# Performance work log

Measured on AMD Instinct MI355X. Metric: run time of the kernel, lower is better.

Reference implementation:

```python
import jax, jax.numpy as jnp
import numpy as np

LN_EPS = 1e-5


def setup_inputs() -> dict:
    key = jax.random.key(0)
    ks = jax.random.split(key, 12)
    B, T, U, H, V = 4, 512, 128, 512, 41
    src = jax.random.normal(ks[0], (B, T, H), dtype=jnp.float32)
    tgt = jax.random.normal(ks[1], (B, U, H), dtype=jnp.float32)
    src_len = jax.random.randint(ks[2], (B,), 1, T + 1, dtype=jnp.int32)
    tgt_len = jax.random.randint(ks[3], (B,), 1, U + 1, dtype=jnp.int32)
    s = 1.0 / np.sqrt(H)
    W1 = jax.random.uniform(ks[4], (H, H), jnp.float32, -s, s)
    b1 = jax.random.uniform(ks[5], (H,), jnp.float32, -s, s)
    W2 = jax.random.uniform(ks[6], (H, H), jnp.float32, -s, s)
    b2 = jax.random.uniform(ks[7], (H,), jnp.float32, -s, s)
    ln_g = jnp.ones((H,), jnp.float32)
    ln_b = jnp.zeros((H,), jnp.float32)
    Wl = jax.random.uniform(ks[8], (H, V), jnp.float32, -s, s)
    bl = jax.random.uniform(ks[9], (V,), jnp.float32, -s, s)
    return dict(source_encodings=src, source_lengths=src_len,
                target_encodings=tgt, target_lengths=tgt_len,
                W1=W1, b1=b1, W2=W2, b2=b2, ln_g=ln_g, ln_b=ln_b,
                Wl=Wl, bl=bl)


def _f_target(tgt, W1, b1, W2, b2, ln_g, ln_b):
    h = jax.nn.gelu(tgt @ W1 + b1, approximate=False)  # exact GELU (torch default)
    h = h @ W2 + b2
    mu = jnp.mean(h, axis=-1, keepdims=True)
    var = jnp.var(h, axis=-1, keepdims=True)
    return (h - mu) * jax.lax.rsqrt(var + LN_EPS) * ln_g + ln_b


def reference(source_encodings, source_lengths, target_encodings, target_lengths,
              W1, b1, W2, b2, ln_g, ln_b, Wl, bl):
    tgt = _f_target(target_encodings, W1, b1, W2, b2, ln_g, ln_b)  # [B,U,H]
    # joint broadcast add: [B,T,1,H] + [B,1,U,H] -> [B,T,U,H]
    joint = source_encodings[:, :, None, :] + tgt[:, None, :, :]
    act = jnp.tanh(joint)
    out = act @ Wl + bl  # [B,T,U,V]
    return out, source_lengths, target_lengths
```

## Files before the change

kernel.cpp:

```cpp
#include <hip/hip_runtime.h>
#include <math.h>

#define Bb 4
#define Tt 512
#define Uu 128
#define Hh 512
#define Vv 41

typedef __attribute__((ext_vector_type(8))) short short8;
typedef __attribute__((ext_vector_type(4))) float f32x4;
typedef __attribute__((ext_vector_type(2))) float v2f;

__device__ __forceinline__ unsigned pack_bf16_rne(float hi, float lo) {
    unsigned xh = __float_as_uint(hi); xh += 0x7fffu + ((xh >> 16) & 1u);
    unsigned xl = __float_as_uint(lo); xl += 0x7fffu + ((xl >> 16) & 1u);
    return __builtin_amdgcn_perm(xh, xl, 0x07060302);
}

__device__ __forceinline__ unsigned short bf16_rne(float v) {
    unsigned x = __float_as_uint(v);
    x += 0x7fffu + ((x >> 16) & 1u);
    return (unsigned short)(x >> 16);
}

__device__ __forceinline__ unsigned tanh2_pack(float x0, float x1) {
    v2f xc;
    xc.x = __builtin_amdgcn_fmed3f(x0, -3.0f, 3.0f);
    xc.y = __builtin_amdgcn_fmed3f(x1, -3.0f, 3.0f);
    v2f t = xc * xc;
    v2f p = t * (v2f){-0.00140725f, -0.00140725f} + (v2f){0.0288922f, 0.0288922f};
    p = p * t + (v2f){-0.2177528f, -0.2177528f};
    p = p * t + (v2f){0.9707868f, 0.9707868f};
    v2f g = xc * p;
    return __builtin_amdgcn_perm(__float_as_uint(g.y), __float_as_uint(g.x), 0x07060302);
}

__global__ __launch_bounds__(256) void prep_pack(
    const float* __restrict__ W1, const float* __restrict__ W2,
    const float* __restrict__ Wl,
    unsigned short* __restrict__ Wp1, unsigned short* __restrict__ Wp2,
    unsigned short* __restrict__ Wpl,
    const int* __restrict__ sl, const int* __restrict__ tl,
    float* __restrict__ lenDst)
{
    __shared__ float T[64][65];
    const int bid = blockIdx.x, tid = threadIdx.x;

    if (bid == 135 && tid < 2 * Bb) {
        lenDst[tid] = (tid < Bb) ? (float)sl[tid] : (float)tl[tid - Bb];
    }

    const float* Wsrc; unsigned short* Wdst; int k0, n0, isWl;
    if (bid < 64)       { Wsrc = W1; Wdst = Wp1; k0 = (bid >> 3) * 64; n0 = (bid & 7) * 64; isWl = 0; }
    else if (bid < 128) { Wsrc = W2; Wdst = Wp2; k0 = ((bid - 64) >> 3) * 64; n0 = ((bid - 64) & 7) * 64; isWl = 0; }
    else                { Wsrc = Wl; Wdst = Wpl; k0 = (bid - 128) * 64; n0 = 0; isWl = 1; }

    #pragma unroll
    for (int i = 0; i < 16; ++i) {
        int idx = i * 256 + tid;
        int kk = idx >> 6, nn = idx & 63;
        float v;
        if (isWl) v = (nn < Vv) ? Wl[(k0 + kk) * Vv + nn] : 0.0f;
        else      v = Wsrc[(size_t)(k0 + kk) * 512 + n0 + nn];
        T[kk][nn] = v;
    }
    __syncthreads();

    #pragma unroll
    for (int i = 0; i < 2; ++i) {
        int task = i * 256 + tid;
        int nn = task & 63, kg = task >> 6;
        if (isWl && nn >= 48) continue;
        int n = n0 + nn, k = k0 + kg * 8;
        float e[8];
        #pragma unroll
        for (int j = 0; j < 8; ++j) e[j] = T[kg * 8 + j][nn];
        uint4 pk;
        pk.x = pack_bf16_rne(e[1], e[0]);
        pk.y = pack_bf16_rne(e[3], e[2]);
        pk.z = pack_bf16_rne(e[5], e[4]);
        pk.w = pack_bf16_rne(e[7], e[6]);
        int ntg = n >> 4, ncol = n & 15;
        int ks = (k >> 5) & 15, quad = (k >> 3) & 3;
        int lane = quad * 16 + ncol;
        *(uint4*)(Wdst + (size_t)((ntg * 16 + ks) * 64 + lane) * 8) = pk;
    }
}

__global__ __launch_bounds__(1024) void target_kernel(
    const float* __restrict__ tgt,
    const unsigned short* __restrict__ Wp1, const float* __restrict__ b1,
    const unsigned short* __restrict__ Wp2, const float* __restrict__ b2,
    const float* __restrict__ ln_g, const float* __restrict__ ln_b,
    float* __restrict__ tgtPf)
{
    __shared__ unsigned short At[16][520];
    __shared__ float Ct[16][516];

    const int tid = threadIdx.x;
    const int lane = tid & 63, wave = tid >> 6;
    const int ncol = lane & 15, quad = lane >> 4;
    const int r0 = blockIdx.x * 16;

    {
        const float4* t4 = (const float4*)(tgt + (size_t)r0 * Hh);
        #pragma unroll
        for (int j = 0; j < 2; ++j) {
            int fi = tid + j * 1024;
            int row = fi >> 7, c4 = fi & 127;
            float4 v = t4[fi];
            uint2 pk;
            pk.x = pack_bf16_rne(v.y, v.x);
            pk.y = pack_bf16_rne(v.w, v.z);
            *(uint2*)&At[row][c4 * 4] = pk;
        }
    }
    __syncthreads();

    f32x4 acc[2];
    acc[0] = (f32x4){0.f, 0.f, 0.f, 0.f};
    acc[1] = (f32x4){0.f, 0.f, 0.f, 0.f};

    const unsigned short* bp1 = Wp1 + (size_t)(wave * 2) * 8192 + lane * 8;
    const unsigned short* bp2 = Wp2 + (size_t)(wave * 2) * 8192 + lane * 8;

    {
        short8 cb0 = *(const short8*)(bp1);
        short8 cb1 = *(const short8*)(bp1 + 8192);
        #pragma unroll
        for (int ks = 0; ks < 16; ++ks) {
            short8 nb0, nb1;
            if (ks < 15) {
                nb0 = *(const short8*)(bp1 + (ks + 1) * 512);
                nb1 = *(const short8*)(bp1 + 8192 + (ks + 1) * 512);
            }
            short8 af = *(const short8*)&At[ncol][ks * 32 + quad * 8];
            acc[0] = __builtin_amdgcn_mfma_f32_16x16x32_bf16(af, cb0, acc[0], 0, 0, 0);
            acc[1] = __builtin_amdgcn_mfma_f32_16x16x32_bf16(af, cb1, acc[1], 0, 0, 0);
            cb0 = nb0; cb1 = nb1;
        }
    }
    __syncthreads();

    #pragma unroll
    for (int nt = 0; nt < 2; ++nt) {
        int n = wave * 32 + nt * 16 + ncol;
        float bias = b1[n];
        #pragma unroll
        for (int r = 0; r < 4; ++r) {
            float v = acc[nt][r] + bias;
            float g = 0.5f * v * (1.0f + erff(v * 0.70710678118654752f));
            At[quad * 4 + r][n] = bf16_rne(g);
        }
        acc[nt] = (f32x4){0.f, 0.f, 0.f, 0.f};
    }
    __syncthreads();

    {
        short8 cb0 = *(const short8*)(bp2);
        short8 cb1 = *(const short8*)(bp2 + 8192);
        #pragma unroll
        for (int ks = 0; ks < 16; ++ks) {
            short8 nb0, nb1;
            if (ks < 15) {
                nb0 = *(const short8*)(bp2 + (ks + 1) * 512);
                nb1 = *(const short8*)(bp2 + 8192 + (ks + 1) * 512);
            }
            short8 af = *(const short8*)&At[ncol][ks * 32 + quad * 8];
            acc[0] = __builtin_amdgcn_mfma_f32_16x16x32_bf16(af, cb0, acc[0], 0, 0, 0);
            acc[1] = __builtin_amdgcn_mfma_f32_16x16x32_bf16(af, cb1, acc[1], 0, 0, 0);
            cb0 = nb0; cb1 = nb1;
        }
    }

    #pragma unroll
    for (int nt = 0; nt < 2; ++nt) {
        int n = wave * 32 + nt * 16 + ncol;
        float bias = b2[n];
        #pragma unroll
        for (int r = 0; r < 4; ++r)
            Ct[quad * 4 + r][n] = acc[nt][r] + bias;
    }
    __syncthreads();

    {
        const int row = wave;
        const float2* cr2 = (const float2*)&Ct[row][0];
        float2 vv[4];
        float s = 0.f, q = 0.f;
        #pragma unroll
        for (int j = 0; j < 4; ++j) {
            float2 v = cr2[lane + 64 * j];
            vv[j] = v;
            s += v.x + v.y;
            q += v.x * v.x + v.y * v.y;
        }
        #pragma unroll
        for (int off = 32; off > 0; off >>= 1) {
            s += __shfl_xor(s, off, 64);
            q += __shfl_xor(q, off, 64);
        }
        float mu = s * (1.0f / Hh);
        float rs = rsqrtf(q * (1.0f / Hh) - mu * mu + 1e-5f);
        int r = r0 + row;
        int bb = r >> 7, u = r & 127;
        float* obase = tgtPf + (size_t)bb * 65536 + u * 8;
        #pragma unroll
        for (int j = 0; j < 4; ++j) {
            int k2 = lane + 64 * j;
            int k = k2 * 2;
            float2 g2 = ((const float2*)ln_g)[k2];
            float2 bv = ((const float2*)ln_b)[k2];
            float2 o;
            o.x = (vv[j].x - mu) * rs * g2.x + bv.x;
            o.y = (vv[j].y - mu) * rs * g2.y + bv.y;
            *(float2*)(obase + ((k >> 3) << 10) + (k & 7)) = o;
        }
    }
}

__global__ __launch_bounds__(256) void joint_mfma(
    const float* __restrict__ src, const float* __restrict__ tgtPf,
    const unsigned short* __restrict__ Wpl, const float* __restrict__ bl,
    float* __restrict__ out)
{
    __shared__ float srcl[2 * Hh];

    const int t0 = blockIdx.x * 2, b = blockIdx.y, uh = blockIdx.z;
    const int tid = threadIdx.x;
    const int lane = tid & 63, wave = tid >> 6;
    const int ncol = lane & 15, quad = lane >> 4;

    const float4* s4 = (const float4*)(src + ((size_t)(b * Tt + t0)) * Hh);
    ((float4*)srcl)[tid] = s4[tid];

    const int u0 = uh * 64 + (wave & 1) * 32 + ncol;
    const float* pA = tgtPf + (size_t)b * 65536 + u0 * 8;
    const unsigned short* bp = Wpl + lane * 8;

    float4 a0 = *(const float4*)(pA + quad * 1024);
    float4 a1 = *(const float4*)(pA + quad * 1024 + 4);
    float4 c0 = *(const float4*)(pA + quad * 1024 + 128);
    float4 c1 = *(const float4*)(pA + quad * 1024 + 132);

    float bln[3];
    #pragma unroll
    for (int nt = 0; nt < 3; ++nt) {
        int n = nt * 16 + ncol;
        bln[nt] = (n < Vv) ? bl[n] : 0.0f;
    }

    f32x4 acc[2][3];
    #pragma unroll
    for (int mi = 0; mi < 2; ++mi)
        #pragma unroll
        for (int nt = 0; nt < 3; ++nt)
            acc[mi][nt] = (f32x4){0.f, 0.f, 0.f, 0.f};

    __syncthreads();

    const float* srow = srcl + (wave >> 1) * Hh;

    #pragma unroll 4
    for (int ks = 0; ks < 16; ++ks) {
        float4 na0, na1, nc0, nc1;
        if (ks < 15) {
            const float* pn = pA + ((ks + 1) * 4 + quad) * 1024;
            na0 = *(const float4*)(pn);
            na1 = *(const float4*)(pn + 4);
            nc0 = *(const float4*)(pn + 128);
            nc1 = *(const float4*)(pn + 132);
        }
        const float* sp = srow + ks * 32 + quad * 8;
        float4 sA = *(const float4*)(sp);
        float4 sB = *(const float4*)(sp + 4);

        union { uint4 u; short8 s; } f0, f1;
        f0.u.x = tanh2_pack(sA.x + a0.x, sA.y + a0.y);
        f0.u.y = tanh2_pack(sA.z + a0.z, sA.w + a0.w);
        f0.u.z = tanh2_pack(sB.x + a1.x, sB.y + a1.y);
        f0.u.w = tanh2_pack(sB.z + a1.z, sB.w + a1.w);
        f1.u.x = tanh2_pack(sA.x + c0.x, sA.y + c0.y);
        f1.u.y = tanh2_pack(sA.z + c0.z, sA.w + c0.w);
        f1.u.z = tanh2_pack(sB.x + c1.x, sB.y + c1.y);
        f1.u.w = tanh2_pack(sB.z + c1.z, sB.w + c1.w);

        #pragma unroll
        for (int nt = 0; nt < 3; ++nt) {
            short8 bfr = *(const short8*)(bp + (nt * 16 + ks) * 512);
            acc[0][nt] = __builtin_amdgcn_mfma_f32_16x16x32_bf16(f0.s, bfr, acc[0][nt], 0, 0, 0);
            acc[1][nt] = __builtin_amdgcn_mfma_f32_16x16x32_bf16(f1.s, bfr, acc[1][nt], 0, 0, 0);
        }
        a0 = na0; a1 = na1; c0 = nc0; c1 = nc1;
    }

    const int t = t0 + (wave >> 1);
    const int ub = uh * 64 + (wave & 1) * 32;
    float* ob = out + ((size_t)(b * Tt + t)) * Uu * Vv;
    #pragma unroll
    for (int mi = 0; mi < 2; ++mi) {
        #pragma unroll
        for (int nt = 0; nt < 3; ++nt) {
            int n = nt * 16 + ncol;
            if (n < Vv) {
                #pragma unroll
                for (int r = 0; r < 4; ++r) {
                    int m = ub + mi * 16 + quad * 4 + r;
                    ob[m * Vv + n] = acc[mi][nt][r] + bln[nt];
                }
            }
        }
    }
}

extern "C" void kernel_launch(void* const* d_in, const int* in_sizes, int n_in,
                              void* d_out, int out_size, void* d_ws, size_t ws_size,
                              hipStream_t stream)
{
    const float* src  = (const float*)d_in[0];
    const int*   slen = (const int*)  d_in[1];
    const float* tgt  = (const float*)d_in[2];
    const int*   tlen = (const int*)  d_in[3];
    const float* W1   = (const float*)d_in[4];
    const float* b1   = (const float*)d_in[5];
    const float* W2   = (const float*)d_in[6];
    const float* b2   = (const float*)d_in[7];
    const float* ln_g = (const float*)d_in[8];
    const float* ln_b = (const float*)d_in[9];
    const float* Wl   = (const float*)d_in[10];
    const float* bl   = (const float*)d_in[11];

    float* out = (float*)d_out;
    float* tgtPf = (float*)d_ws;
    unsigned short* Wp1 = (unsigned short*)((char*)d_ws + 1048576);
    unsigned short* Wp2 = (unsigned short*)((char*)d_ws + 1048576 + 524288);
    unsigned short* Wpl = (unsigned short*)((char*)d_ws + 2097152);

    hipLaunchKernelGGL(prep_pack, dim3(136), dim3(256), 0, stream,
                       W1, W2, Wl, Wp1, Wp2, Wpl,
                       slen, tlen, out + (size_t)Bb * Tt * Uu * Vv);
    hipLaunchKernelGGL(target_kernel, dim3(Bb * Uu / 16), dim3(1024), 0, stream,
                       tgt, Wp1, b1, Wp2, b2, ln_g, ln_b, tgtPf);
    hipLaunchKernelGGL(joint_mfma, dim3(Tt / 2, Bb, 2), dim3(256), 0, stream,
                       src, tgtPf, Wpl, bl, out);
}
```

Measured before the change: 144.4 us.

## Split target MLP into parallel GEMM and layernorm kernels, prefetch joint operands

```diff
diff --git a/kernel.cpp b/kernel.cpp
--- a/kernel.cpp
+++ b/kernel.cpp
@@ -37,19 +37,45 @@
 
 __global__ __launch_bounds__(256) void prep_pack(
     const float* __restrict__ W1, const float* __restrict__ W2,
-    const float* __restrict__ Wl,
+    const float* __restrict__ Wl, const float* __restrict__ tgt,
     unsigned short* __restrict__ Wp1, unsigned short* __restrict__ Wp2,
-    unsigned short* __restrict__ Wpl,
+    unsigned short* __restrict__ Wpl, unsigned short* __restrict__ tgtA,
     const int* __restrict__ sl, const int* __restrict__ tl,
     float* __restrict__ lenDst)
 {
-    __shared__ float T[64][65];
+    __shared__ __align__(16) char smem[16640];
     const int bid = blockIdx.x, tid = threadIdx.x;
 
-    if (bid == 135 && tid < 2 * Bb) {
+    if (bid >= 136) {
+        unsigned short (*At)[520] = (unsigned short (*)[520])smem;
+        const int rt = bid - 136;
+        const float4* t4 = (const float4*)(tgt + (size_t)rt * 16 * Hh);
+        #pragma unroll
+        for (int j = 0; j < 8; ++j) {
+            int fi = j * 256 + tid;
+            int row = fi >> 7, c4 = fi & 127;
+            float4 v = t4[fi];
+            uint2 pk;
+            pk.x = pack_bf16_rne(v.y, v.x);
+            pk.y = pack_bf16_rne(v.w, v.z);
+            *(uint2*)&At[row][c4 * 4] = pk;
+        }
+        __syncthreads();
+        #pragma unroll
+        for (int i = 0; i < 4; ++i) {
+            int chunk = i * 256 + tid;
+            int ks = chunk >> 6, l = chunk & 63;
+            int q = l >> 4, nc = l & 15;
+            short8 v = *(const short8*)&At[nc][ks * 32 + q * 8];
+            *(short8*)(tgtA + ((size_t)(rt * 16 + ks) * 64 + l) * 8) = v;
+        }
+        return;
+    }
+
+    if (bid == 135 && tid < 2 * Bb)
         lenDst[tid] = (tid < Bb) ? (float)sl[tid] : (float)tl[tid - Bb];
-    }
-
+
+    float (*T)[65] = (float (*)[65])smem;
     const float* Wsrc; unsigned short* Wdst; int k0, n0, isWl;
     if (bid < 64)       { Wsrc = W1; Wdst = Wp1; k0 = (bid >> 3) * 64; n0 = (bid & 7) * 64; isWl = 0; }
     else if (bid < 128) { Wsrc = W2; Wdst = Wp2; k0 = ((bid - 64) >> 3) * 64; n0 = ((bid - 64) & 7) * 64; isWl = 0; }
@@ -87,136 +113,135 @@
     }
 }
 
-__global__ __launch_bounds__(1024) void target_kernel(
-    const float* __restrict__ tgt,
+__global__ __launch_bounds__(128) void gemm_t1(
+    const unsigned short* __restrict__ tgtA,
     const unsigned short* __restrict__ Wp1, const float* __restrict__ b1,
+    unsigned short* __restrict__ h1A)
+{
+    __shared__ unsigned short At[16][72];
+    const int nb = blockIdx.x, rt = blockIdx.y;
+    const int tid = threadIdx.x, lane = tid & 63, w = tid >> 6;
+    const int ncol = lane & 15, quad = lane >> 4;
+    const int nt0 = nb * 4 + w * 2;
+
+    const unsigned short* ap = tgtA + ((size_t)rt * 1024 + lane) * 8;
+    const unsigned short* bp = Wp1 + (size_t)lane * 8;
+
+    f32x4 acc0 = (f32x4){0.f,0.f,0.f,0.f}, acc1 = (f32x4){0.f,0.f,0.f,0.f};
+    short8 ac  = *(const short8*)(ap);
+    short8 b0c = *(const short8*)(bp + (size_t)nt0 * 8192);
+    short8 b1c = *(const short8*)(bp + (size_t)(nt0 + 1) * 8192);
+
+    #pragma unroll
+    for (int ks = 0; ks < 16; ++ks) {
+        short8 an, b0n, b1n;
+        if (ks < 15) {
+            an  = *(const short8*)(ap + (ks + 1) * 512);
+            b0n = *(const short8*)(bp + (size_t)nt0 * 8192 + (ks + 1) * 512);
+            b1n = *(const short8*)(bp + (size_t)(nt0 + 1) * 8192 + (ks + 1) * 512);
+        }
+        acc0 = __builtin_amdgcn_mfma_f32_16x16x32_bf16(ac, b0c, acc0, 0, 0, 0);
+        acc1 = __builtin_amdgcn_mfma_f32_16x16x32_bf16(ac, b1c, acc1, 0, 0, 0);
+        ac = an; b0c = b0n; b1c = b1n;
+    }
+
+    #pragma unroll
+    for (int nt = 0; nt < 2; ++nt) {
+        int n = nb * 64 + w * 32 + nt * 16 + ncol;
+        float bias = b1[n];
+        f32x4 A = nt ? acc1 : acc0;
+        #pragma unroll
+        for (int r = 0; r < 4; ++r) {
+            float v = A[r] + bias;
+            float g = 0.5f * v * (1.0f + erff(v * 0.70710678118654752f));
+            At[quad * 4 + r][w * 32 + nt * 16 + ncol] = bf16_rne(g);
+        }
+    }
+    __syncthreads();
+
+    {
+        int g2 = w, l = lane;
+        short8 v = *(const short8*)&At[l & 15][g2 * 32 + (l >> 4) * 8];
+        int ksg = nb * 2 + g2;
+        *(short8*)(h1A + ((size_t)(rt * 16 + ksg) * 64 + l) * 8) = v;
+    }
+}
+
+__global__ __launch_bounds__(128) void gemm_t2(
+    const unsigned short* __restrict__ h1A,
     const unsigned short* __restrict__ Wp2, const float* __restrict__ b2,
-    const float* __restrict__ ln_g, const float* __restrict__ ln_b,
-    float* __restrict__ tgtPf)
-{
-    __shared__ unsigned short At[16][520];
-    __shared__ float Ct[16][516];
-
-    const int tid = threadIdx.x;
-    const int lane = tid & 63, wave = tid >> 6;
+    float* __restrict__ h2)
+{
+    const int nb = blockIdx.x, rt = blockIdx.y;
+    const int tid = threadIdx.x, lane = tid & 63, w = tid >> 6;
     const int ncol = lane & 15, quad = lane >> 4;
-    const int r0 = blockIdx.x * 16;
-
-    {
-        const float4* t4 = (const float4*)(tgt + (size_t)r0 * Hh);
-        #pragma unroll
-        for (int j = 0; j < 2; ++j) {
-            int fi = tid + j * 1024;
-            int row = fi >> 7, c4 = fi & 127;
-            float4 v = t4[fi];
-            uint2 pk;
-            pk.x = pack_bf16_rne(v.y, v.x);
-            pk.y = pack_bf16_rne(v.w, v.z);
-            *(uint2*)&At[row][c4 * 4] = pk;
-        }
-    }
-    __syncthreads();
-
-    f32x4 acc[2];
-    acc[0] = (f32x4){0.f, 0.f, 0.f, 0.f};
-    acc[1] = (f32x4){0.f, 0.f, 0.f, 0.f};
-
-    const unsigned short* bp1 = Wp1 + (size_t)(wave * 2) * 8192 + lane * 8;
-    const unsigned short* bp2 = Wp2 + (size_t)(wave * 2) * 8192 + lane * 8;
-
-    {
-        short8 cb0 = *(const short8*)(bp1);
-        short8 cb1 = *(const short8*)(bp1 + 8192);
-        #pragma unroll
-        for (int ks = 0; ks < 16; ++ks) {
-            short8 nb0, nb1;
-            if (ks < 15) {
-                nb0 = *(const short8*)(bp1 + (ks + 1) * 512);
-                nb1 = *(const short8*)(bp1 + 8192 + (ks + 1) * 512);
-            }
-            short8 af = *(const short8*)&At[ncol][ks * 32 + quad * 8];
-            acc[0] = __builtin_amdgcn_mfma_f32_16x16x32_bf16(af, cb0, acc[0], 0, 0, 0);
-            acc[1] = __builtin_amdgcn_mfma_f32_16x16x32_bf16(af, cb1, acc[1], 0, 0, 0);
-            cb0 = nb0; cb1 = nb1;
-        }
-    }
-    __syncthreads();
+    const int nt0 = nb * 4 + w * 2;
+
+    const unsigned short* ap = h1A + ((size_t)rt * 1024 + lane) * 8;
+    const unsigned short* bp = Wp2 + (size_t)lane * 8;
+
+    f32x4 acc0 = (f32x4){0.f,0.f,0.f,0.f}, acc1 = (f32x4){0.f,0.f,0.f,0.f};
+    short8 ac  = *(const short8*)(ap);
+    short8 b0c = *(const short8*)(bp + (size_t)nt0 * 8192);
+    short8 b1c = *(const short8*)(bp + (size_t)(nt0 + 1) * 8192);
+
+    #pragma unroll
+    for (int ks = 0; ks < 16; ++ks) {
+        short8 an, b0n, b1n;
+        if (ks < 15) {
+            an  = *(const short8*)(ap + (ks + 1) * 512);
+            b0n = *(const short8*)(bp + (size_t)nt0 * 8192 + (ks + 1) * 512);
+            b1n = *(const short8*)(bp + (size_t)(nt0 + 1) * 8192 + (ks + 1) * 512);
+        }
+        acc0 = __builtin_amdgcn_mfma_f32_16x16x32_bf16(ac, b0c, acc0, 0, 0, 0);
+        acc1 = __builtin_amdgcn_mfma_f32_16x16x32_bf16(ac, b1c, acc1, 0, 0, 0);
+        ac = an; b0c = b0n; b1c = b1n;
+    }
 
     #pragma unroll
     for (int nt = 0; nt < 2; ++nt) {
-        int n = wave * 32 + nt * 16 + ncol;
-        float bias = b1[n];
-        #pragma unroll
-        for (int r = 0; r < 4; ++r) {
-            float v = acc[nt][r] + bias;
-            float g = 0.5f * v * (1.0f + erff(v * 0.70710678118654752f));
-            At[quad * 4 + r][n] = bf16_rne(g);
-        }
-        acc[nt] = (f32x4){0.f, 0.f, 0.f, 0.f};
-    }
-    __syncthreads();
-
-    {
-        short8 cb0 = *(const short8*)(bp2);
-        short8 cb1 = *(const short8*)(bp2 + 8192);
-        #pragma unroll
-        for (int ks = 0; ks < 16; ++ks) {
-            short8 nb0, nb1;
-            if (ks < 15) {
-                nb0 = *(const short8*)(bp2 + (ks + 1) * 512);
-                nb1 = *(const short8*)(bp2 + 8192 + (ks + 1) * 512);
-            }
-            short8 af = *(const short8*)&At[ncol][ks * 32 + quad * 8];
-            acc[0] = __builtin_amdgcn_mfma_f32_16x16x32_bf16(af, cb0, acc[0], 0, 0, 0);
-            acc[1] = __builtin_amdgcn_mfma_f32_16x16x32_bf16(af, cb1, acc[1], 0, 0, 0);
-            cb0 = nb0; cb1 = nb1;
-        }
-    }
-
-    #pragma unroll
-    for (int nt = 0; nt < 2; ++nt) {
-        int n = wave * 32 + nt * 16 + ncol;
+        int n = nb * 64 + w * 32 + nt * 16 + ncol;
         float bias = b2[n];
+        f32x4 A = nt ? acc1 : acc0;
         #pragma unroll
         for (int r = 0; r < 4; ++r)
-            Ct[quad * 4 + r][n] = acc[nt][r] + bias;
-    }
-    __syncthreads();
-
-    {
-        const int row = wave;
-        const float2* cr2 = (const float2*)&Ct[row][0];
-        float2 vv[4];
-        float s = 0.f, q = 0.f;
-        #pragma unroll
-        for (int j = 0; j < 4; ++j) {
-            float2 v = cr2[lane + 64 * j];
-            vv[j] = v;
-            s += v.x + v.y;
-            q += v.x * v.x + v.y * v.y;
-        }
-        #pragma unroll
-        for (int off = 32; off > 0; off >>= 1) {
-            s += __shfl_xor(s, off, 64);
-            q += __shfl_xor(q, off, 64);
-        }
-        float mu = s * (1.0f / Hh);
-        float rs = rsqrtf(q * (1.0f / Hh) - mu * mu + 1e-5f);
-        int r = r0 + row;
-        int bb = r >> 7, u = r & 127;
-        float* obase = tgtPf + (size_t)bb * 65536 + u * 8;
-        #pragma unroll
-        for (int j = 0; j < 4; ++j) {
-            int k2 = lane + 64 * j;
-            int k = k2 * 2;
-            float2 g2 = ((const float2*)ln_g)[k2];
-            float2 bv = ((const float2*)ln_b)[k2];
-            float2 o;
-            o.x = (vv[j].x - mu) * rs * g2.x + bv.x;
-            o.y = (vv[j].y - mu) * rs * g2.y + bv.y;
-            *(float2*)(obase + ((k >> 3) << 10) + (k & 7)) = o;
-        }
-    }
+            h2[(size_t)(rt * 16 + quad * 4 + r) * 512 + n] = A[r] + bias;
+    }
+}
+
+__global__ __launch_bounds__(256) void ln_kernel(
+    const float* __restrict__ h2, const float* __restrict__ ln_g,
+    const float* __restrict__ ln_b, float* __restrict__ tgtPf)
+{
+    const int r = blockIdx.x * 4 + (threadIdx.x >> 6);
+    const int lane = threadIdx.x & 63;
+    const float4* row4 = (const float4*)(h2 + (size_t)r * Hh);
+    float4 v0 = row4[lane], v1 = row4[lane + 64];
+    float s = v0.x + v0.y + v0.z + v0.w + v1.x + v1.y + v1.z + v1.w;
+    float q = v0.x*v0.x + v0.y*v0.y + v0.z*v0.z + v0.w*v0.w
+            + v1.x*v1.x + v1.y*v1.y + v1.z*v1.z + v1.w*v1.w;
+    #pragma unroll
+    for (int off = 32; off > 0; off >>= 1) {
+        s += __shfl_xor(s, off, 64);
+        q += __shfl_xor(q, off, 64);
+    }
+    float mu = s * (1.0f / Hh);
+    float rs = rsqrtf(q * (1.0f / Hh) - mu * mu + 1e-5f);
+
+    float4 g0 = ((const float4*)ln_g)[lane], g1 = ((const float4*)ln_g)[lane + 64];
+    float4 be0 = ((const float4*)ln_b)[lane], be1 = ((const float4*)ln_b)[lane + 64];
+    float4 o0, o1;
+    o0.x = (v0.x - mu) * rs * g0.x + be0.x;  o0.y = (v0.y - mu) * rs * g0.y + be0.y;
+    o0.z = (v0.z - mu) * rs * g0.z + be0.z;  o0.w = (v0.w - mu) * rs * g0.w + be0.w;
+    o1.x = (v1.x - mu) * rs * g1.x + be1.x;  o1.y = (v1.y - mu) * rs * g1.y + be1.y;
+    o1.z = (v1.z - mu) * rs * g1.z + be1.z;  o1.w = (v1.w - mu) * rs * g1.w + be1.w;
+
+    const int bb = r >> 7, u = r & 127;
+    float* ob = tgtPf + (size_t)bb * 65536 + u * 8;
+    int k0 = lane * 4;
+    *(float4*)(ob + (k0 >> 3) * 1024 + (k0 & 7)) = o0;
+    int k1 = lane * 4 + 256;
+    *(float4*)(ob + (k1 >> 3) * 1024 + (k1 & 7)) = o1;
 }
 
 __global__ __launch_bounds__(256) void joint_mfma(
@@ -236,44 +261,47 @@
 
     const int u0 = uh * 64 + (wave & 1) * 32 + ncol;
     const float* pA = tgtPf + (size_t)b * 65536 + u0 * 8;
-    const unsigned short* bp = Wpl + lane * 8;
+    const unsigned short* bp = Wpl + (size_t)lane * 8;
 
     float4 a0 = *(const float4*)(pA + quad * 1024);
     float4 a1 = *(const float4*)(pA + quad * 1024 + 4);
     float4 c0 = *(const float4*)(pA + quad * 1024 + 128);
     float4 c1 = *(const float4*)(pA + quad * 1024 + 132);
-
-    float bln[3];
+    short8 B0 = *(const short8*)(bp);
+    short8 B1 = *(const short8*)(bp + 8192);
+    short8 B2 = *(const short8*)(bp + 16384);
+
+    f32x4 acc[2][3];
     #pragma unroll
     for (int nt = 0; nt < 3; ++nt) {
         int n = nt * 16 + ncol;
-        bln[nt] = (n < Vv) ? bl[n] : 0.0f;
-    }
-
-    f32x4 acc[2][3];
-    #pragma unroll
-    for (int mi = 0; mi < 2; ++mi)
-        #pragma unroll
-        for (int nt = 0; nt < 3; ++nt)
-            acc[mi][nt] = (f32x4){0.f, 0.f, 0.f, 0.f};
+        float bv = (n < Vv) ? bl[n] : 0.0f;
+        acc[0][nt] = (f32x4){bv, bv, bv, bv};
+        acc[1][nt] = (f32x4){bv, bv, bv, bv};
+    }
 
     __syncthreads();
-
     const float* srow = srcl + (wave >> 1) * Hh;
+    float4 sA = *(const float4*)(srow + quad * 8);
+    float4 sB = *(const float4*)(srow + quad * 8 + 4);
 
     #pragma unroll 4
     for (int ks = 0; ks < 16; ++ks) {
-        float4 na0, na1, nc0, nc1;
+        float4 na0, na1, nc0, nc1, nsA, nsB;
+        short8 nB0, nB1, nB2;
         if (ks < 15) {
             const float* pn = pA + ((ks + 1) * 4 + quad) * 1024;
             na0 = *(const float4*)(pn);
             na1 = *(const float4*)(pn + 4);
             nc0 = *(const float4*)(pn + 128);
             nc1 = *(const float4*)(pn + 132);
-        }
-        const float* sp = srow + ks * 32 + quad * 8;
-        float4 sA = *(const float4*)(sp);
-        float4 sB = *(const float4*)(sp + 4);
+            nB0 = *(const short8*)(bp + (ks + 1) * 512);
+            nB1 = *(const short8*)(bp + 8192 + (ks + 1) * 512);
+            nB2 = *(const short8*)(bp + 16384 + (ks + 1) * 512);
+            const float* spn = srow + (ks + 1) * 32 + quad * 8;
+            nsA = *(const float4*)(spn);
+            nsB = *(const float4*)(spn + 4);
+        }
 
         union { uint4 u; short8 s; } f0, f1;
         f0.u.x = tanh2_pack(sA.x + a0.x, sA.y + a0.y);
@@ -285,13 +313,16 @@
         f1.u.z = tanh2_pack(sB.x + c1.x, sB.y + c1.y);
         f1.u.w = tanh2_pack(sB.z + c1.z, sB.w + c1.w);
 
-        #pragma unroll
-        for (int nt = 0; nt < 3; ++nt) {
-            short8 bfr = *(const short8*)(bp + (nt * 16 + ks) * 512);
-            acc[0][nt] = __builtin_amdgcn_mfma_f32_16x16x32_bf16(f0.s, bfr, acc[0][nt], 0, 0, 0);
-            acc[1][nt] = __builtin_amdgcn_mfma_f32_16x16x32_bf16(f1.s, bfr, acc[1][nt], 0, 0, 0);
-        }
+        acc[0][0] = __builtin_amdgcn_mfma_f32_16x16x32_bf16(f0.s, B0, acc[0][0], 0, 0, 0);
+        acc[1][0] = __builtin_amdgcn_mfma_f32_16x16x32_bf16(f1.s, B0, acc[1][0], 0, 0, 0);
+        acc[0][1] = __builtin_amdgcn_mfma_f32_16x16x32_bf16(f0.s, B1, acc[0][1], 0, 0, 0);
+        acc[1][1] = __builtin_amdgcn_mfma_f32_16x16x32_bf16(f1.s, B1, acc[1][1], 0, 0, 0);
+        acc[0][2] = __builtin_amdgcn_mfma_f32_16x16x32_bf16(f0.s, B2, acc[0][2], 0, 0, 0);
+        acc[1][2] = __builtin_amdgcn_mfma_f32_16x16x32_bf16(f1.s, B2, acc[1][2], 0, 0, 0);
+
         a0 = na0; a1 = na1; c0 = nc0; c1 = nc1;
+        B0 = nB0; B1 = nB1; B2 = nB2;
+        sA = nsA; sB = nsB;
     }
 
     const int t = t0 + (wave >> 1);
@@ -306,7 +337,7 @@
                 #pragma unroll
                 for (int r = 0; r < 4; ++r) {
                     int m = ub + mi * 16 + quad * 4 + r;
-                    ob[m * Vv + n] = acc[mi][nt][r] + bln[nt];
+                    ob[m * Vv + n] = acc[mi][nt][r];
                 }
             }
         }
@@ -331,16 +362,24 @@
     const float* bl   = (const float*)d_in[11];
 
     float* out = (float*)d_out;
-    float* tgtPf = (float*)d_ws;
-    unsigned short* Wp1 = (unsigned short*)((char*)d_ws + 1048576);
-    unsigned short* Wp2 = (unsigned short*)((char*)d_ws + 1048576 + 524288);
-    unsigned short* Wpl = (unsigned short*)((char*)d_ws + 2097152);
-
-    hipLaunchKernelGGL(prep_pack, dim3(136), dim3(256), 0, stream,
-                       W1, W2, Wl, Wp1, Wp2, Wpl,
+    char* ws = (char*)d_ws;
+    float*          tgtPf = (float*)(ws);
+    unsigned short* Wp1   = (unsigned short*)(ws + 1048576);
+    unsigned short* Wp2   = (unsigned short*)(ws + 1572864);
+    unsigned short* Wpl   = (unsigned short*)(ws + 2097152);
+    unsigned short* tgtA  = (unsigned short*)(ws + 2162688);
+    unsigned short* h1A   = (unsigned short*)(ws + 2686976);
+    float*          h2    = (float*)(ws + 3211264);
+
+    hipLaunchKernelGGL(prep_pack, dim3(168), dim3(256), 0, stream,
+                       W1, W2, Wl, tgt, Wp1, Wp2, Wpl, tgtA,
                        slen, tlen, out + (size_t)Bb * Tt * Uu * Vv);
-    hipLaunchKernelGGL(target_kernel, dim3(Bb * Uu / 16), dim3(1024), 0, stream,
-                       tgt, Wp1, b1, Wp2, b2, ln_g, ln_b, tgtPf);
+    hipLaunchKernelGGL(gemm_t1, dim3(8, 32), dim3(128), 0, stream,
+                       tgtA, Wp1, b1, h1A);
+    hipLaunchKernelGGL(gemm_t2, dim3(8, 32), dim3(128), 0, stream,
+                       h1A, Wp2, b2, h2);
+    hipLaunchKernelGGL(ln_kernel, dim3(128), dim3(256), 0, stream,
+                       h2, ln_g, ln_b, tgtPf);
     hipLaunchKernelGGL(joint_mfma, dim3(Tt / 2, Bb, 2), dim3(256), 0, stream,
                        src, tgtPf, Wpl, bl, out);
 }
```

New measurement: 141.5 us. -2.0%, faster.
